# Kernel tuning notes

Hardware: AMD Instinct MI355X
Metric: run time of the kernel (lower is better)

Reference implementation:

```python
import jax, jax.numpy as jnp
import numpy as np


def setup_inputs() -> dict:
    key = jax.random.key(0)
    k1, k2, k3 = jax.random.split(key, 3)
    B, H, W, C = 16, 112, 112, 128
    t1 = jax.random.normal(k1, (B, H, W, C), dtype=jnp.float32)
    t2 = jax.random.normal(k2, (B, H, W, C), dtype=jnp.float32)
    # shared 1x1 conv: kernel (1,1,2,1) -> two scalars, plus bias
    w = jax.random.normal(k3, (2,), dtype=jnp.float32)
    b = jnp.zeros((1,), dtype=jnp.float32)
    return {"t1": t1, "t2": t2, "w": w, "b": b}


def reference(t1, t2, w, b):
    # Per-channel loop of [concat(t1_i, t2_i) -> 1x1 conv(2->1, shared weights) -> relu]
    # is mathematically relu(w0*t1 + w1*t2 + b), broadcast over all channels.
    return jax.nn.relu(w[0] * t1 + w[1] * t2 + b[0])
```

## Files before the change

kernel.cpp:

```cpp
#include <hip/hip_runtime.h>


__global__ void __launch_bounds__(256) fused_merge_relu_f4(
    const float4* __restrict__ t1,
    const float4* __restrict__ t2,
    float4* __restrict__ out,
    const float* __restrict__ w,
    const float* __restrict__ b,
    int n4)
{
    const float w0 = w[0];
    const float w1 = w[1];
    const float bb = b[0];

    int stride = gridDim.x * blockDim.x;
    for (int i = blockIdx.x * blockDim.x + threadIdx.x; i < n4; i += stride) {
        float4 a = t1[i];
        float4 c = t2[i];
        float4 r;
        r.x = fmaxf(fmaf(w0, a.x, fmaf(w1, c.x, bb)), 0.0f);
        r.y = fmaxf(fmaf(w0, a.y, fmaf(w1, c.y, bb)), 0.0f);
        r.z = fmaxf(fmaf(w0, a.z, fmaf(w1, c.z, bb)), 0.0f);
        r.w = fmaxf(fmaf(w0, a.w, fmaf(w1, c.w, bb)), 0.0f);
        out[i] = r;
    }
}

__global__ void __launch_bounds__(256) fused_merge_relu_tail(
    const float* __restrict__ t1,
    const float* __restrict__ t2,
    float* __restrict__ out,
    const float* __restrict__ w,
    const float* __restrict__ b,
    int start, int n)
{
    int i = start + blockIdx.x * blockDim.x + threadIdx.x;
    if (i < n) {
        out[i] = fmaxf(fmaf(w[0], t1[i], fmaf(w[1], t2[i], b[0])), 0.0f);
    }
}

extern "C" void kernel_launch(void* const* d_in, const int* in_sizes, int n_in,
                              void* d_out, int out_size, void* d_ws, size_t ws_size,
                              hipStream_t stream) {
    const float* t1 = (const float*)d_in[0];
    const float* t2 = (const float*)d_in[1];
    const float* w  = (const float*)d_in[2];
    const float* b  = (const float*)d_in[3];
    float* out = (float*)d_out;

    const int n  = out_size;
    const int n4 = n / 4;
    const int tail = n - n4 * 4;

    const int block = 256;
    int grid = (n4 + block - 1) / block;
    if (grid > 2048) grid = 2048;

    fused_merge_relu_f4<<<grid, block, 0, stream>>>(
        (const float4*)t1, (const float4*)t2, (float4*)out, w, b, n4);

    if (tail > 0) {
        int tg = (tail + block - 1) / block;
        fused_merge_relu_tail<<<tg, block, 0, stream>>>(t1, t2, out, w, b, n4 * 4, n);
    }
}
```

Baseline: 252.4 us.

## Process four float4s per thread with full grid and nontemporal stores

Replaces the grid-stride loop capped at 2048 blocks with a non-looping kernel where each thread handles four float4 elements strided by 256, issuing all eight loads before computing. The launch grid now covers the whole tensor, and output writes use nontemporal stores to avoid polluting cache. The aim is more memory-level parallelism per thread and less streaming-write cache traffic, at the cost of many more blocks to launch and a bounds-checked slow path for the last block.

```diff
diff --git a/kernel.cpp b/kernel.cpp
--- a/kernel.cpp
+++ b/kernel.cpp
@@ -1,10 +1,12 @@
 #include <hip/hip_runtime.h>
 
 
-__global__ void __launch_bounds__(256) fused_merge_relu_f4(
-    const float4* __restrict__ t1,
-    const float4* __restrict__ t2,
-    float4* __restrict__ out,
+typedef float v4f __attribute__((ext_vector_type(4)));
+
+__global__ void __launch_bounds__(256) fused_merge_relu_f4x4(
+    const v4f* __restrict__ t1,
+    const v4f* __restrict__ t2,
+    v4f* __restrict__ out,
     const float* __restrict__ w,
     const float* __restrict__ b,
     int n4)
@@ -13,16 +15,44 @@
     const float w1 = w[1];
     const float bb = b[0];
 
-    int stride = gridDim.x * blockDim.x;
-    for (int i = blockIdx.x * blockDim.x + threadIdx.x; i < n4; i += stride) {
-        float4 a = t1[i];
-        float4 c = t2[i];
-        float4 r;
-        r.x = fmaxf(fmaf(w0, a.x, fmaf(w1, c.x, bb)), 0.0f);
-        r.y = fmaxf(fmaf(w0, a.y, fmaf(w1, c.y, bb)), 0.0f);
-        r.z = fmaxf(fmaf(w0, a.z, fmaf(w1, c.z, bb)), 0.0f);
-        r.w = fmaxf(fmaf(w0, a.w, fmaf(w1, c.w, bb)), 0.0f);
-        out[i] = r;
+    const int base = blockIdx.x * 1024 + threadIdx.x;
+
+    if (base + 768 < n4) {
+        v4f a0 = t1[base];
+        v4f a1 = t1[base + 256];
+        v4f a2 = t1[base + 512];
+        v4f a3 = t1[base + 768];
+        v4f c0 = t2[base];
+        v4f c1 = t2[base + 256];
+        v4f c2 = t2[base + 512];
+        v4f c3 = t2[base + 768];
+
+        v4f r0, r1, r2, r3;
+        #pragma unroll
+        for (int k = 0; k < 4; ++k) {
+            r0[k] = fmaxf(fmaf(w0, a0[k], fmaf(w1, c0[k], bb)), 0.0f);
+            r1[k] = fmaxf(fmaf(w0, a1[k], fmaf(w1, c1[k], bb)), 0.0f);
+            r2[k] = fmaxf(fmaf(w0, a2[k], fmaf(w1, c2[k], bb)), 0.0f);
+            r3[k] = fmaxf(fmaf(w0, a3[k], fmaf(w1, c3[k], bb)), 0.0f);
+        }
+
+        __builtin_nontemporal_store(r0, &out[base]);
+        __builtin_nontemporal_store(r1, &out[base + 256]);
+        __builtin_nontemporal_store(r2, &out[base + 512]);
+        __builtin_nontemporal_store(r3, &out[base + 768]);
+    } else {
+        for (int j = 0; j < 4; ++j) {
+            int i = base + j * 256;
+            if (i < n4) {
+                v4f a = t1[i];
+                v4f c = t2[i];
+                v4f r;
+                #pragma unroll
+                for (int k = 0; k < 4; ++k)
+                    r[k] = fmaxf(fmaf(w0, a[k], fmaf(w1, c[k], bb)), 0.0f);
+                __builtin_nontemporal_store(r, &out[i]);
+            }
+        }
     }
 }
 
@@ -54,11 +84,11 @@
     const int tail = n - n4 * 4;
 
     const int block = 256;
-    int grid = (n4 + block - 1) / block;
-    if (grid > 2048) grid = 2048;
+    const int per_block = block * 4;
+    int grid = (n4 + per_block - 1) / per_block;
 
-    fused_merge_relu_f4<<<grid, block, 0, stream>>>(
-        (const float4*)t1, (const float4*)t2, (float4*)out, w, b, n4);
+    fused_merge_relu_f4x4<<<grid, block, 0, stream>>>(
+        (const v4f*)t1, (const v4f*)t2, (v4f*)out, w, b, n4);
 
     if (tail > 0) {
         int tg = (tail + block - 1) / block;
```

Measured after the change: 253.0 us. Within noise of the previous version (+0.2%).
